# Kernel tuning notes

Measured on AMD Instinct MI355X. Metric: run time of the kernel, lower is better.

The kernel has to match this reference:

```python
import jax, jax.numpy as jnp
import numpy as np

HEADS = 4
HID = 32
IN_CH = 3
N = 50000
E = 800000


def setup_inputs() -> dict:
    key = jax.random.key(0)
    ks = jax.random.split(key, 16)
    d1 = HEADS * HID  # 128
    s = 0.1
    inp = {
        'x': jax.random.normal(ks[0], (N, IN_CH), jnp.float32),
        'edge_index': jax.random.randint(ks[1], (2, E), 0, N, jnp.int64),
        # layer 1: in=3 -> heads*hid
        'W1': jax.random.normal(ks[2], (IN_CH, d1), jnp.float32) * s,
        'as1': jax.random.normal(ks[3], (HEADS, HID), jnp.float32) * s,
        'ad1': jax.random.normal(ks[4], (HEADS, HID), jnp.float32) * s,
        'b1': jnp.zeros((d1,), jnp.float32),
        # layer 2: 128 -> 128
        'W2': jax.random.normal(ks[5], (d1, d1), jnp.float32) * s,
        'as2': jax.random.normal(ks[6], (HEADS, HID), jnp.float32) * s,
        'ad2': jax.random.normal(ks[7], (HEADS, HID), jnp.float32) * s,
        'b2': jnp.zeros((d1,), jnp.float32),
        # layer 3: 128 -> 128
        'W3': jax.random.normal(ks[8], (d1, d1), jnp.float32) * s,
        'as3': jax.random.normal(ks[9], (HEADS, HID), jnp.float32) * s,
        'ad3': jax.random.normal(ks[10], (HEADS, HID), jnp.float32) * s,
        'b3': jnp.zeros((d1,), jnp.float32),
        # classifier: 128 -> 1
        'cW': jax.random.normal(ks[11], (d1, 1), jnp.float32) * s,
        'cb': jnp.zeros((1,), jnp.float32),
    }
    return inp


def _gat_layer(x, src, dst, n, W, a_s, a_d, b):
    """PyG GATConv (concat=True, negative_slope=0.2, self-loops already added)."""
    xp = (x @ W).reshape(n, HEADS, HID)              # [N,H,C]
    al_s = jnp.einsum('nhc,hc->nh', xp, a_s)          # [N,H]
    al_d = jnp.einsum('nhc,hc->nh', xp, a_d)          # [N,H]
    e = jax.nn.leaky_relu(al_s[src] + al_d[dst], 0.2)  # [E',H]
    emax = jax.ops.segment_max(e, dst, num_segments=n)  # segment softmax over dst
    ex = jnp.exp(e - emax[dst])
    den = jax.ops.segment_sum(ex, dst, num_segments=n)
    alpha = ex / (den[dst] + 1e-16)                   # [E',H]
    msg = xp[src] * alpha[:, :, None]                 # [E',H,C]
    out = jax.ops.segment_sum(msg, dst, num_segments=n)  # [N,H,C]
    return out.reshape(n, HEADS * HID) + b


def reference(x, edge_index, W1, as1, ad1, b1, W2, as2, ad2, b2, W3, as3, ad3, b3, cW, cb):
    n = x.shape[0]
    loops = jnp.arange(n, dtype=edge_index.dtype)
    src = jnp.concatenate([edge_index[0], loops])     # add self-loops (PyG default)
    dst = jnp.concatenate([edge_index[1], loops])
    h = jax.nn.elu(_gat_layer(x, src, dst, n, W1, as1, ad1, b1))
    h = jax.nn.elu(_gat_layer(h, src, dst, n, W2, as2, ad2, b2))
    h = jax.nn.elu(_gat_layer(h, src, dst, n, W3, as3, ad3, b3))
    logits = (h @ cW + cb)[:, 0]                      # [N]
    return jax.nn.sigmoid(logits)                     # eval mode output
```

## Files before the change

### kernel.cpp

```cpp
#include <hip/hip_runtime.h>
#include <math.h>

typedef unsigned int uint_t;
typedef __attribute__((ext_vector_type(8))) short bf16x8;
typedef __attribute__((ext_vector_type(4))) float f32x4;

#define BK_SHIFT 7
#define BK_NODES 128
#define MAXBK 512
#define PART_CHUNK 4096
#define SLAB 4096

__device__ __forceinline__ float lrelu(float x){ return x > 0.f ? x : 0.2f*x; }
__device__ __forceinline__ float sel4(float a, float b, float c, float d, int h){
    return h==0 ? a : (h==1 ? b : (h==2 ? c : d));
}
__device__ __forceinline__ float wsum(float v){
    #pragma unroll
    for (int m = 1; m < 64; m <<= 1) v += __shfl_xor(v, m);
    return v;
}
__device__ __forceinline__ uint_t pack_bf2(float a, float b){
    uint_t ua = __float_as_uint(a); uint_t ub = __float_as_uint(b);
    ua += 0x7FFFu + ((ua >> 16) & 1u);
    ub += 0x7FFFu + ((ub >> 16) & 1u);
    return (ua >> 16) | (ub & 0xFFFF0000u);
}
__device__ __forceinline__ float bflo(uint_t u){ return __uint_as_float(u << 16); }
__device__ __forceinline__ float bfhi(uint_t u){ return __uint_as_float(u & 0xFFFF0000u); }
__device__ __forceinline__ bf16x8 mk_bf8(uint4 u){
    bf16x8 r;
    r[0]=(short)(u.x & 0xFFFFu); r[1]=(short)(u.x >> 16);
    r[2]=(short)(u.y & 0xFFFFu); r[3]=(short)(u.y >> 16);
    r[4]=(short)(u.z & 0xFFFFu); r[5]=(short)(u.z >> 16);
    r[6]=(short)(u.w & 0xFFFFu); r[7]=(short)(u.w >> 16);
    return r;
}


__global__ void zero_kernel(int* __restrict__ gcursor){
    gcursor[threadIdx.x] = 0;
}

__global__ __launch_bounds__(256) void partition_slab(
        const int* __restrict__ ei, int E, int N,
        int* __restrict__ gcursor, uint_t* __restrict__ pairbuf, int NBK){
    __shared__ int hist[MAXBK];
    __shared__ int sA[MAXBK];
    __shared__ int destadj[MAXBK];
    __shared__ int cnt2[MAXBK];
    __shared__ uint_t staged[PART_CHUNK];
    __shared__ unsigned short sbk[PART_CHUNK];
    int t = threadIdx.x;
    int base = blockIdx.x * PART_CHUNK;
    int total = E + N;
    int cnt = total - base; if (cnt > PART_CHUNK) cnt = PART_CHUNK; if (cnt < 0) cnt = 0;

    for (int i = t; i < MAXBK; i += 256){ hist[i] = 0; cnt2[i] = 0; }
    __syncthreads();
    for (int i = t; i < cnt; i += 256){
        int idx = base + i;
        int d = (idx < E) ? ei[E + idx] : (idx - E);
        atomicAdd(&hist[d >> BK_SHIFT], 1);
    }
    __syncthreads();
    sA[t] = hist[t]; sA[t + 256] = hist[t + 256];
    __syncthreads();
    for (int off = 1; off < MAXBK; off <<= 1){
        int i0 = t, i1 = t + 256;
        int a0 = sA[i0] + ((i0 >= off) ? sA[i0 - off] : 0);
        int a1 = sA[i1] + ((i1 >= off) ? sA[i1 - off] : 0);
        __syncthreads();
        sA[i0] = a0; sA[i1] = a1;
        __syncthreads();
    }
    for (int b = t; b < NBK; b += 256){
        int c = hist[b];
        int gstart = (b == 0) ? 0 : sA[b - 1];
        int rbase = c > 0 ? atomicAdd(&gcursor[b], c) : 0;
        destadj[b] = b * SLAB + rbase - gstart;
        cnt2[b] = gstart;
    }
    __syncthreads();
    for (int i = t; i < cnt; i += 256){
        int idx = base + i;
        int d, s;
        if (idx < E){ s = ei[idx]; d = ei[E + idx]; }
        else        { s = d = idx - E; }
        int b = d >> BK_SHIFT;
        int pos = atomicAdd(&cnt2[b], 1);
        staged[pos] = (uint_t)s | ((uint_t)(d & (BK_NODES - 1)) << 25);
        sbk[pos] = (unsigned short)b;
    }
    __syncthreads();
    for (int p = t; p < cnt; p += 256){
        int b = (int)sbk[p];
        pairbuf[destadj[b] + p] = staged[p];
    }
}

__global__ __launch_bounds__(256) void sort2_slab(
        const uint_t* __restrict__ pairbuf, const int* __restrict__ gcursor,
        int* __restrict__ indptr, int* __restrict__ indend,
        int* __restrict__ srcs, int N, int NBK){
    int b = blockIdx.x;
    int cnt = gcursor[b];
    int base = b * SLAB;
    int nb = b << BK_SHIFT;
    __shared__ int nh[BK_NODES];
    __shared__ int noff[BK_NODES];
    __shared__ int outb[SLAB];
    int t = threadIdx.x;
    if (t < BK_NODES) nh[t] = 0;
    __syncthreads();
    for (int i = t; i < cnt; i += 256){
        uint_t pr = pairbuf[base + i];
        atomicAdd(&nh[(int)(pr >> 25)], 1);
    }
    __syncthreads();
    if (t < BK_NODES) noff[t] = nh[t];
    __syncthreads();
    for (int off = 1; off < BK_NODES; off <<= 1){
        int u = 0;
        if (t < BK_NODES && t >= off) u = noff[t - off];
        __syncthreads();
        if (t < BK_NODES) noff[t] += u;
        __syncthreads();
    }
    if (t < BK_NODES){
        int node = nb + t;
        if (node < N){
            int excl = noff[t] - nh[t];
            indptr[node] = base + excl;
            indend[node] = base + noff[t];
        }
        nh[t] = noff[t] - nh[t];
    }
    __syncthreads();
    for (int i = t; i < cnt; i += 256){
        uint_t pr = pairbuf[base + i];
        int pos = atomicAdd(&nh[(int)(pr >> 25)], 1);
        outb[pos] = (int)(pr & 0x1FFFFFFu);
    }
    __syncthreads();
    for (int i = t; i < cnt; i += 256) srcs[base + i] = outb[i];
}

__global__ __launch_bounds__(128) void linear_al(
        const float* __restrict__ in, const float* __restrict__ W,
        const float* __restrict__ as_, const float* __restrict__ ad_,
        uint_t* __restrict__ xp16, float* __restrict__ als, float* __restrict__ ald,
        int N, int K){
    __shared__ float hs[8 * 3];
    int t = threadIdx.x;
    int base = blockIdx.x * 8;
    int rows = N - base; if (rows > 8) rows = 8;
    for (int idx = t; idx < rows * K; idx += 128){
        int r = idx / K, k = idx - r * K;
        hs[r * K + k] = in[(size_t)(base + r) * K + k];
    }
    __syncthreads();
    float acc[8] = {0.f,0.f,0.f,0.f,0.f,0.f,0.f,0.f};
    for (int k = 0; k < K; ++k){
        float w = W[k * 128 + t];
        #pragma unroll
        for (int r = 0; r < 8; ++r) acc[r] += hs[r * K + k] * w;
    }
    float asv = as_[t], adv = ad_[t];
    for (int r = 0; r < rows; ++r){
        int row = base + r;
        float v = acc[r];
        float vo = __shfl_xor(v, 1);
        if (!(t & 1)) xp16[(size_t)row * 64 + (t >> 1)] = pack_bf2(v, vo);
        float vs = v * asv, vd = v * adv;
        #pragma unroll
        for (int m = 16; m >= 1; m >>= 1){
            vs += __shfl_xor(vs, m);
            vd += __shfl_xor(vd, m);
        }
        if ((t & 31) == 0){
            int h = t >> 5;
            als[row * 4 + h] = vs;
            ald[row * 4 + h] = vd;
        }
    }
}

__global__ __launch_bounds__(256) void wpack_kernel(
        const float* __restrict__ W2, const float* __restrict__ W3,
        uint_t* __restrict__ B2, uint_t* __restrict__ B3){
    int idx = blockIdx.x * 256 + threadIdx.x;
    const float* W = (idx < 8192) ? W2 : W3;
    uint_t* Bp = (idx < 8192) ? B2 : B3;
    int i = idx & 8191;
    int u = i & 3, c = (i >> 2) & 15, kg = (i >> 6) & 3, kb = (i >> 8) & 3, cb = (i >> 10) & 7;
    int k = kb * 32 + kg * 8 + 2 * u;
    int col = cb * 16 + c;
    Bp[i] = pack_bf2(W[k * 128 + col], W[(k + 1) * 128 + col]);
}

__global__ __launch_bounds__(256) void gemm_mfma(
        const uint_t* __restrict__ h16, const uint_t* __restrict__ bpack,
        const float* __restrict__ as_, const float* __restrict__ ad_,
        uint_t* __restrict__ xp16, float* __restrict__ als, float* __restrict__ ald,
        int N){
    int w = threadIdx.x >> 6;
    int l = threadIdx.x & 63;
    int stripe = blockIdx.x * 4 + w;
    int base = stripe * 16;
    if (base >= N) return;
    int r16 = l & 15;
    int kg  = l >> 4;
    int row = base + r16;
    int rowc = row < N ? row : N - 1;

    bf16x8 afr[4];
    const uint4* hrow = (const uint4*)(h16 + (size_t)rowc * 64);
    #pragma unroll
    for (int kb = 0; kb < 4; ++kb) afr[kb] = mk_bf8(hrow[kb * 4 + kg]);

    f32x4 acc[8];
    #pragma unroll
    for (int cb = 0; cb < 8; ++cb) acc[cb] = (f32x4){0.f, 0.f, 0.f, 0.f};

    const uint4* bp = (const uint4*)bpack;
    #pragma unroll
    for (int cb = 0; cb < 8; ++cb){
        #pragma unroll
        for (int kb = 0; kb < 4; ++kb){
            bf16x8 bfr = mk_bf8(bp[((cb * 4 + kb) * 4 + kg) * 16 + r16]);
            acc[cb] = __builtin_amdgcn_mfma_f32_16x16x32_bf16(afr[kb], bfr, acc[cb], 0, 0, 0);
        }
    }

    #pragma unroll
    for (int reg = 0; reg < 4; ++reg){
        int ro = base + kg * 4 + reg;
        bool wr = (ro < N) && ((r16 & 1) == 0);
        #pragma unroll
        for (int cb = 0; cb < 8; ++cb){
            float v  = acc[cb][reg];
            float vo = __shfl_xor(v, 1);
            if (wr) xp16[(size_t)ro * 64 + cb * 8 + (r16 >> 1)] = pack_bf2(v, vo);
        }
        #pragma unroll
        for (int h = 0; h < 4; ++h){
            float a0 = as_[h * 32 + r16],      a1 = as_[h * 32 + 16 + r16];
            float g0 = ad_[h * 32 + r16],      g1 = ad_[h * 32 + 16 + r16];
            float ps = acc[2 * h][reg] * a0 + acc[2 * h + 1][reg] * a1;
            float pd = acc[2 * h][reg] * g0 + acc[2 * h + 1][reg] * g1;
            ps += __shfl_xor(ps, 1); ps += __shfl_xor(ps, 2);
            ps += __shfl_xor(ps, 4); ps += __shfl_xor(ps, 8);
            pd += __shfl_xor(pd, 1); pd += __shfl_xor(pd, 2);
            pd += __shfl_xor(pd, 4); pd += __shfl_xor(pd, 8);
            if (r16 == 0 && ro < N){
                als[(size_t)ro * 4 + h] = ps;
                ald[(size_t)ro * 4 + h] = pd;
            }
        }
    }
}

__global__ __launch_bounds__(256, 8) void gat_agg4(
        const uint_t* __restrict__ xp16, const float4* __restrict__ als,
        const float4* __restrict__ ald,
        const int* __restrict__ indptr, const int* __restrict__ indend,
        const int* __restrict__ srcs,
        const float* __restrict__ bias,
        uint_t* __restrict__ hout, int N, int mode,
        const float* __restrict__ cW, const float* __restrict__ cb,
        float* __restrict__ fout){
    int wid = threadIdx.x >> 6;
    int l   = threadIdx.x & 63;
    int n = blockIdx.x * 4 + wid;
    __shared__ int   ssh[4][64];
    __shared__ float esh[4][64][4];
    if (n >= N) return;

    int beg = indptr[n], end = indend[n];
    float4 ad4 = ald[n];
    int h = l >> 4;

    float d0 = 0.f, d1 = 0.f, d2 = 0.f, d3 = 0.f;
    float ax = 0.f, ay = 0.f;

    for (int cbeg = beg; cbeg < end; cbeg += 64){
        int cnt = end - cbeg; if (cnt > 64) cnt = 64;
        if (l < cnt){
            int s = srcs[cbeg + l];
            ssh[wid][l] = s;
            float4 a4 = als[s];
            float p0 = __expf(lrelu(a4.x + ad4.x));
            float p1 = __expf(lrelu(a4.y + ad4.y));
            float p2 = __expf(lrelu(a4.z + ad4.z));
            float p3 = __expf(lrelu(a4.w + ad4.w));
            *((float4*)&esh[wid][l][0]) = make_float4(p0, p1, p2, p3);
            d0 += p0; d1 += p1; d2 += p2; d3 += p3;
        }
        __builtin_amdgcn_wave_barrier();

        int j = 0;
        for (; j + 16 <= cnt; j += 16){
            int ss[16]; float ww[16]; uint_t uu[16];
            #pragma unroll
            for (int q = 0; q < 16; ++q){ ss[q] = ssh[wid][j+q]; ww[q] = esh[wid][j+q][h]; }
            #pragma unroll
            for (int q = 0; q < 16; ++q) uu[q] = xp16[(size_t)ss[q] * 64 + l];
            #pragma unroll
            for (int q = 0; q < 16; ++q){
                ax = fmaf(bflo(uu[q]), ww[q], ax);
                ay = fmaf(bfhi(uu[q]), ww[q], ay);
            }
        }
        for (; j + 8 <= cnt; j += 8){
            int ss[8]; float ww[8]; uint_t uu[8];
            #pragma unroll
            for (int q = 0; q < 8; ++q){ ss[q] = ssh[wid][j+q]; ww[q] = esh[wid][j+q][h]; }
            #pragma unroll
            for (int q = 0; q < 8; ++q) uu[q] = xp16[(size_t)ss[q] * 64 + l];
            #pragma unroll
            for (int q = 0; q < 8; ++q){
                ax = fmaf(bflo(uu[q]), ww[q], ax);
                ay = fmaf(bfhi(uu[q]), ww[q], ay);
            }
        }
        for (; j < cnt; ++j){
            int s = ssh[wid][j];
            float w = esh[wid][j][h];
            uint_t u = xp16[(size_t)s * 64 + l];
            ax = fmaf(bflo(u), w, ax);
            ay = fmaf(bfhi(u), w, ay);
        }
    }

    d0 = wsum(d0); d1 = wsum(d1); d2 = wsum(d2); d3 = wsum(d3);

    float dh = sel4(d0, d1, d2, d3, h);
    float inv = 1.f / (dh + 1e-16f);
    float2 b2 = ((const float2*)bias)[l];
    float vx = ax * inv + b2.x;
    float vy = ay * inv + b2.y;
    vx = vx > 0.f ? vx : (__expf(vx) - 1.f);
    vy = vy > 0.f ? vy : (__expf(vy) - 1.f);

    if (mode == 0){
        hout[(size_t)n * 64 + l] = pack_bf2(vx, vy);
    } else {
        float2 cw2 = ((const float2*)cW)[l];
        float p = vx * cw2.x + vy * cw2.y;
        p = wsum(p);
        if (l == 0){
            float logit = p + cb[0];
            fout[n] = 1.f / (1.f + __expf(-logit));
        }
    }
}

extern "C" void kernel_launch(void* const* d_in, const int* in_sizes, int n_in,
                              void* d_out, int out_size, void* d_ws, size_t ws_size,
                              hipStream_t stream){
    const float* x   = (const float*)d_in[0];
    const int*   ei  = (const int*)d_in[1];
    const float* W1  = (const float*)d_in[2];
    const float* as1 = (const float*)d_in[3];
    const float* ad1 = (const float*)d_in[4];
    const float* b1  = (const float*)d_in[5];
    const float* W2  = (const float*)d_in[6];
    const float* as2 = (const float*)d_in[7];
    const float* ad2 = (const float*)d_in[8];
    const float* b2  = (const float*)d_in[9];
    const float* W3  = (const float*)d_in[10];
    const float* as3 = (const float*)d_in[11];
    const float* ad3 = (const float*)d_in[12];
    const float* b3  = (const float*)d_in[13];
    const float* cW  = (const float*)d_in[14];
    const float* cb  = (const float*)d_in[15];
    float* out = (float*)d_out;

    int N = in_sizes[0] / 3;
    int E = in_sizes[1] / 2;
    int EN = E + N;
    int NBK = (N + BK_NODES - 1) / BK_NODES;

    char* ws = (char*)d_ws;
    size_t off = 0;
    auto alloc = [&](size_t bytes) -> void* {
        void* p = ws + off;
        off += (bytes + 255) & ~(size_t)255;
        return p;
    };
    int*    indptr  = (int*)alloc((size_t)N * 4);
    int*    indend  = (int*)alloc((size_t)N * 4);
    int*    srcs    = (int*)alloc((size_t)NBK * SLAB * 4);
    uint_t* pairbuf = (uint_t*)alloc((size_t)NBK * SLAB * 4);
    uint_t* XP      = (uint_t*)alloc((size_t)N * 64 * 4);
    uint_t* H16     = (uint_t*)alloc((size_t)N * 64 * 4);
    float*  ALS     = (float*)alloc((size_t)N * 4 * 4);
    float*  ALD     = (float*)alloc((size_t)N * 4 * 4);
    int*    gcursor = (int*)alloc((size_t)MAXBK * 4);
    uint_t* BP2     = (uint_t*)alloc((size_t)8192 * 4);
    uint_t* BP3     = (uint_t*)alloc((size_t)8192 * 4);
    (void)ws_size;

    int pb = (EN + PART_CHUNK - 1) / PART_CHUNK;

    zero_kernel<<<1, MAXBK, 0, stream>>>(gcursor);
    partition_slab<<<pb, 256, 0, stream>>>(ei, E, N, gcursor, pairbuf, NBK);
    sort2_slab<<<NBK, 256, 0, stream>>>(pairbuf, gcursor, indptr, indend, srcs, N, NBK);
    wpack_kernel<<<64, 256, 0, stream>>>(W2, W3, BP2, BP3);

    int ab = (N + 3) / 4;
    int gb = ((N + 15) / 16 + 3) / 4;
    linear_al<<<(N + 7) / 8, 128, 0, stream>>>(x, W1, as1, ad1, XP, ALS, ALD, N, 3);
    gat_agg4<<<ab, 256, 0, stream>>>(XP, (const float4*)ALS, (const float4*)ALD,
                                     indptr, indend, srcs, b1, H16, N, 0, nullptr, nullptr, nullptr);
    gemm_mfma<<<gb, 256, 0, stream>>>(H16, BP2, as2, ad2, XP, ALS, ALD, N);
    gat_agg4<<<ab, 256, 0, stream>>>(XP, (const float4*)ALS, (const float4*)ALD,
                                     indptr, indend, srcs, b2, H16, N, 0, nullptr, nullptr, nullptr);
    gemm_mfma<<<gb, 256, 0, stream>>>(H16, BP3, as3, ad3, XP, ALS, ALD, N);
    gat_agg4<<<ab, 256, 0, stream>>>(XP, (const float4*)ALS, (const float4*)ALD,
                                     indptr, indend, srcs, b3, nullptr, N, 1, cW, cb, out);
}
```

Measured before the change: 217.1 us.

## Fuse weight packing with cursor zeroing, register-cache edges, stage B in LDS

Merges the cursor-zeroing kernel into the weight-packing kernel, which removes one launch. The partition kernel now loads each thread's 16 edges into registers once, so the histogram and scatter passes no longer read edge_index twice. The MFMA GEMM stages the packed B matrix (32 KB) in shared memory per block rather than reading it from global/L2 for every fragment. The tradeoffs are extra register pressure in the partition kernel and an LDS fill plus a block barrier at the start of each GEMM block.

```diff
diff --git a/kernel.cpp b/kernel.cpp
--- a/kernel.cpp
+++ b/kernel.cpp
@@ -37,10 +37,21 @@
     return r;
 }
 
-
-__global__ void zero_kernel(int* __restrict__ gcursor){
-    gcursor[threadIdx.x] = 0;
-}
+__global__ __launch_bounds__(256) void wpack_zero(
+        const float* __restrict__ W2, const float* __restrict__ W3,
+        uint_t* __restrict__ B2, uint_t* __restrict__ B3,
+        int* __restrict__ gcursor){
+    int idx = blockIdx.x * 256 + threadIdx.x;
+    if (idx < MAXBK) gcursor[idx] = 0;
+    const float* W = (idx < 8192) ? W2 : W3;
+    uint_t* Bp = (idx < 8192) ? B2 : B3;
+    int i = idx & 8191;
+    int u = i & 3, c = (i >> 2) & 15, kg = (i >> 6) & 3, kb = (i >> 8) & 3, cb = (i >> 10) & 7;
+    int k = kb * 32 + kg * 8 + 2 * u;
+    int col = cb * 16 + c;
+    Bp[i] = pack_bf2(W[k * 128 + col], W[(k + 1) * 128 + col]);
+}
+
 
 __global__ __launch_bounds__(256) void partition_slab(
         const int* __restrict__ ei, int E, int N,
@@ -56,13 +67,24 @@
     int total = E + N;
     int cnt = total - base; if (cnt > PART_CHUNK) cnt = PART_CHUNK; if (cnt < 0) cnt = 0;
 
+    int sreg[16], dreg[16];
+    #pragma unroll
+    for (int q = 0; q < 16; ++q){
+        int i = t + q * 256;
+        int idx = base + i;
+        int s = 0, d = -1;
+        if (i < cnt){
+            if (idx < E){ s = ei[idx]; d = ei[E + idx]; }
+            else        { s = d = idx - E; }
+        }
+        sreg[q] = s; dreg[q] = d;
+    }
+
     for (int i = t; i < MAXBK; i += 256){ hist[i] = 0; cnt2[i] = 0; }
     __syncthreads();
-    for (int i = t; i < cnt; i += 256){
-        int idx = base + i;
-        int d = (idx < E) ? ei[E + idx] : (idx - E);
-        atomicAdd(&hist[d >> BK_SHIFT], 1);
-    }
+    #pragma unroll
+    for (int q = 0; q < 16; ++q)
+        if (dreg[q] >= 0) atomicAdd(&hist[dreg[q] >> BK_SHIFT], 1);
     __syncthreads();
     sA[t] = hist[t]; sA[t + 256] = hist[t + 256];
     __syncthreads();
@@ -82,15 +104,14 @@
         cnt2[b] = gstart;
     }
     __syncthreads();
-    for (int i = t; i < cnt; i += 256){
-        int idx = base + i;
-        int d, s;
-        if (idx < E){ s = ei[idx]; d = ei[E + idx]; }
-        else        { s = d = idx - E; }
-        int b = d >> BK_SHIFT;
-        int pos = atomicAdd(&cnt2[b], 1);
-        staged[pos] = (uint_t)s | ((uint_t)(d & (BK_NODES - 1)) << 25);
-        sbk[pos] = (unsigned short)b;
+    #pragma unroll
+    for (int q = 0; q < 16; ++q){
+        if (dreg[q] >= 0){
+            int b = dreg[q] >> BK_SHIFT;
+            int pos = atomicAdd(&cnt2[b], 1);
+            staged[pos] = (uint_t)sreg[q] | ((uint_t)(dreg[q] & (BK_NODES - 1)) << 25);
+            sbk[pos] = (unsigned short)b;
+        }
     }
     __syncthreads();
     for (int p = t; p < cnt; p += 256){
@@ -186,24 +207,18 @@
     }
 }
 
-__global__ __launch_bounds__(256) void wpack_kernel(
-        const float* __restrict__ W2, const float* __restrict__ W3,
-        uint_t* __restrict__ B2, uint_t* __restrict__ B3){
-    int idx = blockIdx.x * 256 + threadIdx.x;
-    const float* W = (idx < 8192) ? W2 : W3;
-    uint_t* Bp = (idx < 8192) ? B2 : B3;
-    int i = idx & 8191;
-    int u = i & 3, c = (i >> 2) & 15, kg = (i >> 6) & 3, kb = (i >> 8) & 3, cb = (i >> 10) & 7;
-    int k = kb * 32 + kg * 8 + 2 * u;
-    int col = cb * 16 + c;
-    Bp[i] = pack_bf2(W[k * 128 + col], W[(k + 1) * 128 + col]);
-}
-
 __global__ __launch_bounds__(256) void gemm_mfma(
         const uint_t* __restrict__ h16, const uint_t* __restrict__ bpack,
         const float* __restrict__ as_, const float* __restrict__ ad_,
         uint_t* __restrict__ xp16, float* __restrict__ als, float* __restrict__ ald,
         int N){
+    __shared__ uint4 Bs[2048];
+    int t = threadIdx.x;
+    const uint4* bp4 = (const uint4*)bpack;
+    #pragma unroll
+    for (int q = 0; q < 8; ++q) Bs[t + q * 256] = bp4[t + q * 256];
+    __syncthreads();
+
     int w = threadIdx.x >> 6;
     int l = threadIdx.x & 63;
     int stripe = blockIdx.x * 4 + w;
@@ -223,12 +238,11 @@
     #pragma unroll
     for (int cb = 0; cb < 8; ++cb) acc[cb] = (f32x4){0.f, 0.f, 0.f, 0.f};
 
-    const uint4* bp = (const uint4*)bpack;
     #pragma unroll
     for (int cb = 0; cb < 8; ++cb){
         #pragma unroll
         for (int kb = 0; kb < 4; ++kb){
-            bf16x8 bfr = mk_bf8(bp[((cb * 4 + kb) * 4 + kg) * 16 + r16]);
+            bf16x8 bfr = mk_bf8(Bs[((cb * 4 + kb) * 4 + kg) * 16 + r16]);
             acc[cb] = __builtin_amdgcn_mfma_f32_16x16x32_bf16(afr[kb], bfr, acc[cb], 0, 0, 0);
         }
     }
@@ -404,10 +418,9 @@
 
     int pb = (EN + PART_CHUNK - 1) / PART_CHUNK;
 
-    zero_kernel<<<1, MAXBK, 0, stream>>>(gcursor);
+    wpack_zero<<<64, 256, 0, stream>>>(W2, W3, BP2, BP3, gcursor);
     partition_slab<<<pb, 256, 0, stream>>>(ei, E, N, gcursor, pairbuf, NBK);
     sort2_slab<<<NBK, 256, 0, stream>>>(pairbuf, gcursor, indptr, indend, srcs, N, NBK);
-    wpack_kernel<<<64, 256, 0, stream>>>(W2, W3, BP2, BP3);
 
     int ab = (N + 3) / 4;
     int gb = ((N + 15) / 16 + 3) / 4;
```

After: 206.5 us (median of 2 runs). 4.8% less time.
